# Kernel tuning notes

Hardware: AMD Instinct MI355X
Metric: run time of the kernel (lower is better)

The kernel has to match this reference:

```python
import jax, jax.numpy as jnp
import numpy as np

B, D, T = 32, 6, 2048
FH, ENC, H, CONF, NC, K = 128, 128, 256, 64, 10, 5


def setup_inputs() -> dict:
    key = jax.random.key(0)
    ks = iter(jax.random.split(key, 40))
    n = lambda shape, s=0.05: jax.random.normal(next(ks), shape, dtype=jnp.float32) * s
    inp = {
        'M': jax.random.normal(next(ks), (B, D, T), dtype=jnp.float32),
        # causal conv frontend (4 dilated convs, kernel 5)
        'conv_w0': n((FH, D, K)), 'conv_b0': n((FH,)),
        'conv_w1': n((FH, FH, K)), 'conv_b1': n((FH,)),
        'conv_w2': n((FH, FH, K)), 'conv_b2': n((FH,)),
        'conv_w3': n((FH, FH, K)), 'conv_b3': n((FH,)),
        # encoder projection
        'enc_w': n((ENC, FH)), 'enc_b': n((ENC,)),
        # selective state space
        'A': n((H, H), 0.01), 'ip_w': n((H, ENC)), 'ip_b': n((H,)),
        'state_bias': jnp.zeros((H,), jnp.float32),
        'op_w': n((H, H)), 'op_b': n((H,)),
        # classifier head
        'cls_w1': n((256, H)), 'cls_b1': n((256,)),
        'cls_w2': n((NC, 256)), 'cls_b2': n((NC,)),
        # metanet: 2*D -> 64 -> 128 -> confound_dim
        'mn_w1': n((64, 2 * D)), 'mn_b1': n((64,)),
        'mn_w2': n((128, 64)), 'mn_b2': n((128,)),
        'mn_w3': n((CONF, 128)), 'mn_b3': n((CONF,)),
        # frontdoor: confound_dim -> 128 -> ssm_hidden
        'fd_w1': n((128, CONF)), 'fd_b1': n((128,)),
        'fd_w2': n((H, 128)), 'fd_b2': n((H,)),
    }
    return inp


def _causal_conv(x, w, b, d):
    # x: (B,C,T), w: (O,I,K). pad-left (K-1)*d == pad-both + trim-right in torch code
    y = jax.lax.conv_general_dilated(
        x, w, window_strides=(1,), padding=[((w.shape[2] - 1) * d, 0)],
        rhs_dilation=(d,), dimension_numbers=('NCH', 'OIH', 'NCH'))
    return jax.nn.relu(y + b[None, :, None])


def reference(M, conv_w0, conv_b0, conv_w1, conv_b1, conv_w2, conv_b2, conv_w3, conv_b3,
              enc_w, enc_b, A, ip_w, ip_b, state_bias, op_w, op_b,
              cls_w1, cls_b1, cls_w2, cls_b2,
              mn_w1, mn_b1, mn_w2, mn_b2, mn_w3, mn_b3,
              fd_w1, fd_b1, fd_w2, fd_b2):
    # frontend: 4 causal dilated convs with ReLU
    out = M
    for w, b, d in ((conv_w0, conv_b0, 1), (conv_w1, conv_b1, 2),
                    (conv_w2, conv_b2, 4), (conv_w3, conv_b3, 8)):
        out = _causal_conv(out, w, b, d)
    feat = jnp.einsum('bct,ec->bte', out, enc_w) + enc_b  # (B,T,ENC)
    # SSM: precompute input projection, then sequential scan over T
    u = jnp.einsum('bte,he->bth', feat, ip_w) + ip_b + state_bias  # (B,T,H)

    def step(h, ut):
        h = jax.nn.gelu(h @ A.T + ut, approximate=False)
        return h, h

    h0 = jnp.zeros((M.shape[0], A.shape[0]), M.dtype)
    _, hs = jax.lax.scan(step, h0, jnp.swapaxes(u, 0, 1))  # hs: (T,B,H)
    ssm_out = jnp.einsum('tbh,gh->btg', hs, op_w) + op_b  # (B,T,H)
    pooled = ssm_out.mean(axis=1)  # (B,H)
    logits = jax.nn.relu(pooled @ cls_w1.T + cls_b1) @ cls_w2.T + cls_b2
    # confounder summary: mean & unbiased std over time
    s = jnp.concatenate([M.mean(axis=2), jnp.std(M, axis=2, ddof=1)], axis=1)
    z = jax.nn.relu(s @ mn_w1.T + mn_b1)
    z = jax.nn.relu(z @ mn_w2.T + mn_b2)
    conf_hat = z @ mn_w3.T + mn_b3
    adj = jax.nn.relu(conf_hat @ fd_w1.T + fd_b1) @ fd_w2.T + fd_b2
    corrected = pooled - adj
    return (logits, pooled, corrected, conf_hat)
```

## Files before the change

### kernel.cpp

```cpp
#include <hip/hip_runtime.h>
#include <cmath>


typedef __bf16 bf16_t;
typedef bf16_t bf16x8 __attribute__((ext_vector_type(8)));
typedef float f32x4 __attribute__((ext_vector_type(4)));

__device__ __forceinline__ f32x4 mfma16(bf16x8 a, bf16x8 b, f32x4 c) {
  return __builtin_amdgcn_mfma_f32_16x16x32_bf16(a, b, c, 0, 0, 0);
}

__device__ __forceinline__ float gelu_f(float x) {
  float a = x * 0.70710678118654752440f;
  float z = fabsf(a);
  float t = __builtin_amdgcn_rcpf(1.0f + 0.3275911f * z);
  float p = t * (0.254829592f +
            t * (-0.284496736f +
            t * (1.421413741f +
            t * (-1.453152027f +
            t * 1.061405429f))));
  float e = __expf(-z * z);
  float erf_a = __builtin_copysignf(1.0f - p * e, a);
  return 0.5f * x * (1.0f + erf_a);
}

__global__ void k_prep(const float* __restrict__ w0, const float* __restrict__ w1,
                       const float* __restrict__ w2, const float* __restrict__ w3,
                       const float* __restrict__ ip_w, const float* __restrict__ enc_w,
                       const float* __restrict__ enc_b, const float* __restrict__ ip_b,
                       const float* __restrict__ sbias,
                       bf16_t* __restrict__ wb0, bf16_t* __restrict__ wb1,
                       bf16_t* __restrict__ wb2, bf16_t* __restrict__ wb3,
                       bf16_t* __restrict__ wce, float* __restrict__ bce) {
  int bid = blockIdx.x;
  if (bid >= 976) {
    int idx = (bid - 976) * 256 + threadIdx.x;
    int h = idx >> 7, c = idx & 127;
    float s = 0.f;
    for (int e = 0; e < 128; ++e) s += ip_w[h * 128 + e] * enc_w[e * 128 + c];
    wce[h * 128 + c] = (bf16_t)s;
    if (c == 0) {
      float bv = 0.f;
      for (int e = 0; e < 128; ++e) bv += ip_w[h * 128 + e] * enc_b[e];
      bce[h] = bv + ip_b[h] + sbias[h];
    }
    return;
  }
  int idx = bid * 256 + threadIdx.x;
  if (idx < 128 * 32) {
    int o = idx >> 5, k = idx & 31;
    float v = 0.f;
    if (k < 30) { int i = k / 5, kk = k - i * 5; v = w0[(o * 6 + i) * 5 + kk]; }
    wb0[idx] = (bf16_t)v;
    return;
  }
  int e = idx - 128 * 32;
  if (e < 3 * 5 * 128 * 128) {
    int layer = e / (5 * 128 * 128);
    int r = e - layer * (5 * 128 * 128);
    int ks = r / 16384;
    int o = (r >> 7) & 127;
    int i = r & 127;
    const float* w = layer == 0 ? w1 : layer == 1 ? w2 : w3;
    bf16_t* wb = layer == 0 ? wb1 : layer == 1 ? wb2 : wb3;
    wb[r] = (bf16_t)w[(o * 128 + i) * 5 + ks];
  }
}

__global__ __launch_bounds__(256) void k_conv0(const float* __restrict__ M,
                                               const bf16_t* __restrict__ wb0,
                                               const float* __restrict__ b0,
                                               bf16_t* __restrict__ out) {
  __shared__ float raw[6][136];
  __shared__ bf16_t Xe[128 * 40];
  const int tid = threadIdx.x;
  const int b = blockIdx.y, t0 = blockIdx.x * 128;
  for (int id = tid; id < 6 * 132; id += 256) {
    int i = id / 132, j = id - i * 132;
    int t = t0 - 4 + j;
    raw[i][j] = (t >= 0) ? M[((size_t)b * 6 + i) * 2048 + t] : 0.f;
  }
  __syncthreads();
  for (int id = tid; id < 128 * 32; id += 256) {
    int tl = id >> 5, k = id & 31;
    float v = 0.f;
    if (k < 30) { int i = k / 5, kk = k - i * 5; v = raw[i][tl + kk]; }
    Xe[tl * 40 + k] = (bf16_t)v;
  }
  __syncthreads();
  const int w = tid >> 6, lane = tid & 63, q = lane >> 4, l15 = lane & 15;
  const int k0 = q * 8;
  const f32x4 z4 = {0.f, 0.f, 0.f, 0.f};
  f32x4 acc[2][8];
#pragma unroll
  for (int mt = 0; mt < 2; ++mt)
#pragma unroll
    for (int nt = 0; nt < 8; ++nt) acc[mt][nt] = z4;
  bf16x8 af[2];
#pragma unroll
  for (int mt = 0; mt < 2; ++mt)
    af[mt] = *(const bf16x8*)&Xe[(w * 32 + mt * 16 + l15) * 40 + k0];
#pragma unroll
  for (int nt = 0; nt < 8; ++nt) {
    bf16x8 bf = *(const bf16x8*)&wb0[(nt * 16 + l15) * 32 + k0];
#pragma unroll
    for (int mt = 0; mt < 2; ++mt) acc[mt][nt] = mfma16(af[mt], bf, acc[mt][nt]);
  }
#pragma unroll
  for (int nt = 0; nt < 8; ++nt) {
    const int o = nt * 16 + l15;
    const float bias = b0[o];
#pragma unroll
    for (int mt = 0; mt < 2; ++mt) {
#pragma unroll
      for (int r = 0; r < 4; ++r) {
        int t = t0 + w * 32 + mt * 16 + q * 4 + r;
        float v = acc[mt][nt][r] + bias;
        out[((size_t)b * 2048 + t) * 128 + o] = (bf16_t)(v > 0.f ? v : 0.f);
      }
    }
  }
}

template <int DIL>
__global__ __launch_bounds__(256) void k_conv(const bf16_t* __restrict__ in,
                                              const bf16_t* __restrict__ wb,
                                              const float* __restrict__ bias,
                                              bf16_t* __restrict__ out) {
  __shared__ bf16_t Xs[160 * 136];
  const int tid = threadIdx.x;
  const int b = blockIdx.y, t0 = blockIdx.x * 128;
  const bf16_t* src = in + (size_t)b * 2048 * 128;
  for (int id = tid; id < 160 * 16; id += 256) {
    int r = id >> 4, ck = id & 15;
    int t = t0 + r - 32;
    int4 v = make_int4(0, 0, 0, 0);
    if (t >= 0) v = *(const int4*)(src + (size_t)t * 128 + ck * 8);
    *(int4*)&Xs[r * 136 + ck * 8] = v;
  }
  __syncthreads();
  const int w = tid >> 6, lane = tid & 63, q = lane >> 4, l15 = lane & 15;
  const f32x4 z4 = {0.f, 0.f, 0.f, 0.f};
  f32x4 acc[2][8];
#pragma unroll
  for (int mt = 0; mt < 2; ++mt)
#pragma unroll
    for (int nt = 0; nt < 8; ++nt) acc[mt][nt] = z4;
#pragma unroll
  for (int ks = 0; ks < 5; ++ks) {
    const int shift = (4 - ks) * DIL;
#pragma unroll
    for (int kt = 0; kt < 4; ++kt) {
      const int k0 = kt * 32 + q * 8;
      bf16x8 af[2];
#pragma unroll
      for (int mt = 0; mt < 2; ++mt)
        af[mt] = *(const bf16x8*)&Xs[(32 + w * 32 + mt * 16 + l15 - shift) * 136 + k0];
#pragma unroll
      for (int nt = 0; nt < 8; ++nt) {
        bf16x8 bf = *(const bf16x8*)&wb[((size_t)ks * 128 + nt * 16 + l15) * 128 + k0];
#pragma unroll
        for (int mt = 0; mt < 2; ++mt) acc[mt][nt] = mfma16(af[mt], bf, acc[mt][nt]);
      }
    }
  }
#pragma unroll
  for (int nt = 0; nt < 8; ++nt) {
    const int o = nt * 16 + l15;
    const float bv = bias[o];
#pragma unroll
    for (int mt = 0; mt < 2; ++mt) {
#pragma unroll
      for (int r = 0; r < 4; ++r) {
        int t = t0 + w * 32 + mt * 16 + q * 4 + r;
        float v = acc[mt][nt][r] + bv;
        out[((size_t)b * 2048 + t) * 128 + o] = (bf16_t)(v > 0.f ? v : 0.f);
      }
    }
  }
}

__global__ __launch_bounds__(256) void k_ugemm(const bf16_t* __restrict__ in,
                                               const bf16_t* __restrict__ wce,
                                               const float* __restrict__ bce,
                                               bf16_t* __restrict__ u) {
  __shared__ bf16_t Xs[128 * 136];
  const int tid = threadIdx.x;
  const int b = blockIdx.y, t0 = blockIdx.x * 128, hh = blockIdx.z;
  const bf16_t* src = in + (size_t)b * 2048 * 128;
  for (int id = tid; id < 128 * 16; id += 256) {
    int r = id >> 4, ck = id & 15;
    *(int4*)&Xs[r * 136 + ck * 8] = *(const int4*)(src + (size_t)(t0 + r) * 128 + ck * 8);
  }
  __syncthreads();
  const int w = tid >> 6, lane = tid & 63, q = lane >> 4, l15 = lane & 15;
  const f32x4 z4 = {0.f, 0.f, 0.f, 0.f};
  f32x4 acc[2][8];
#pragma unroll
  for (int mt = 0; mt < 2; ++mt)
#pragma unroll
    for (int nt = 0; nt < 8; ++nt) acc[mt][nt] = z4;
#pragma unroll
  for (int kt = 0; kt < 4; ++kt) {
    const int k0 = kt * 32 + q * 8;
    bf16x8 af[2];
#pragma unroll
    for (int mt = 0; mt < 2; ++mt)
      af[mt] = *(const bf16x8*)&Xs[(w * 32 + mt * 16 + l15) * 136 + k0];
#pragma unroll
    for (int nt = 0; nt < 8; ++nt) {
      bf16x8 bf = *(const bf16x8*)&wce[((size_t)hh * 128 + nt * 16 + l15) * 128 + k0];
#pragma unroll
      for (int mt = 0; mt < 2; ++mt) acc[mt][nt] = mfma16(af[mt], bf, acc[mt][nt]);
    }
  }
#pragma unroll
  for (int nt = 0; nt < 8; ++nt) {
    const int h = hh * 128 + nt * 16 + l15;
    const float bv = bce[h];
#pragma unroll
    for (int mt = 0; mt < 2; ++mt) {
#pragma unroll
      for (int r = 0; r < 4; ++r) {
        int t = t0 + w * 32 + mt * 16 + q * 4 + r;
        u[((size_t)b * 2048 + t) * 256 + h] = (bf16_t)(acc[mt][nt][r] + bv);
      }
    }
  }
}

__global__ __launch_bounds__(1024, 1) void k_scan(const float* __restrict__ Am,
                                                  const bf16_t* __restrict__ u,
                                                  float* __restrict__ hbarOut) {
  __shared__ bf16_t hb[2][256];
  const int b = blockIdx.x;
  const int tid = threadIdx.x;
  const int w = tid >> 6, lane = tid & 63, q = lane >> 4, l15 = lane & 15;
  const int c = w * 16 + l15;

  bf16x8 bfr[8];
#pragma unroll
  for (int kt = 0; kt < 8; ++kt) {
    const float* ap = Am + (size_t)c * 256 + kt * 32 + q * 8;
    f32x4 p0 = *(const f32x4*)ap;
    f32x4 p1 = *(const f32x4*)(ap + 4);
    bf16x8 v;
    v[0] = (bf16_t)p0[0]; v[1] = (bf16_t)p0[1]; v[2] = (bf16_t)p0[2]; v[3] = (bf16_t)p0[3];
    v[4] = (bf16_t)p1[0]; v[5] = (bf16_t)p1[1]; v[6] = (bf16_t)p1[2]; v[7] = (bf16_t)p1[3];
    bfr[kt] = v;
  }
  if (tid < 256) {
    hb[0][tid] = (bf16_t)0.f;
    hb[1][tid] = (bf16_t)0.f;
  }
  const bf16_t* up = u + (size_t)b * 2048 * 256 + c;
  float hbar = 0.f;
  bf16_t ua = up[0];
  bf16_t ub = up[256];
  __syncthreads();

  const f32x4 z4 = {0.f, 0.f, 0.f, 0.f};

#define SCAN_STEP(RD, WR, UREG)                                   \
  {                                                               \
    bf16x8 af[8];                                                 \
    _Pragma("unroll")                                             \
    for (int kt = 0; kt < 8; ++kt)                                \
      af[kt] = *(const bf16x8*)&hb[RD][kt * 32 + q * 8];          \
    float uin = (float)(UREG);                                    \
    f32x4 acc = z4;                                               \
    acc[0] = uin;                                                 \
    _Pragma("unroll")                                             \
    for (int kt = 0; kt < 8; ++kt)                                \
      acc = mfma16(af[kt], bfr[kt], acc);                         \
    __builtin_amdgcn_sched_group_barrier(0x100, 8, 0);            \
    __builtin_amdgcn_sched_group_barrier(0x008, 8, 0);            \
    float g = gelu_f(acc[0]);                                     \
    if (q == 0) hb[WR][c] = (bf16_t)g;                            \
    asm volatile("s_waitcnt lgkmcnt(0)" ::: "memory");            \
    __builtin_amdgcn_s_barrier();                                 \
    __builtin_amdgcn_sched_barrier(0);                            \
    hbar += g;                                                    \
  }

  for (int t = 0; t < 2048; t += 2) {
    bf16_t ua2 = (t + 2 < 2048) ? up[(size_t)(t + 2) * 256] : (bf16_t)0.f;
    SCAN_STEP(0, 1, ua)
    bf16_t ub2 = (t + 3 < 2048) ? up[(size_t)(t + 3) * 256] : (bf16_t)0.f;
    SCAN_STEP(1, 0, ub)
    ua = ua2;
    ub = ub2;
  }
#undef SCAN_STEP

  if (q == 0) hbarOut[b * 256 + c] = hbar * (1.f / 2048.f);
}

__global__ __launch_bounds__(256) void k_post(
    const float* __restrict__ M, const float* __restrict__ hbar,
    const float* __restrict__ w1, const float* __restrict__ b1,
    const float* __restrict__ w2, const float* __restrict__ b2,
    const float* __restrict__ w3, const float* __restrict__ b3,
    const float* __restrict__ f1, const float* __restrict__ fb1,
    const float* __restrict__ f2, const float* __restrict__ fb2,
    const float* __restrict__ op_w, const float* __restrict__ op_b,
    const float* __restrict__ cw1, const float* __restrict__ cb1,
    const float* __restrict__ cw2, const float* __restrict__ cb2,
    float* __restrict__ out) {
  const int b = blockIdx.x, tid = threadIdx.x;
  const int w = tid >> 6, lane = tid & 63;
  __shared__ float s12[12], z1[64], z2[128], ch[64], a1[128], adjs[256];
  __shared__ float hs[256], ps[256], hid[256];
  __shared__ float as_[4], ass_[4];
  for (int c = 0; c < 6; ++c) {
    const float* p = M + ((size_t)b * 6 + c) * 2048;
    float s = 0.f, ss = 0.f;
    for (int t = tid; t < 2048; t += 256) { float v = p[t]; s += v; ss += v * v; }
    for (int o = 32; o > 0; o >>= 1) { s += __shfl_down(s, o, 64); ss += __shfl_down(ss, o, 64); }
    if (lane == 0) { as_[w] = s; ass_[w] = ss; }
    __syncthreads();
    if (tid == 0) {
      s = as_[0] + as_[1] + as_[2] + as_[3];
      ss = ass_[0] + ass_[1] + ass_[2] + ass_[3];
      float mean = s * (1.f / 2048.f);
      float var = (ss - 2048.f * mean * mean) * (1.f / 2047.f);
      if (var < 0.f) var = 0.f;
      s12[c] = mean;
      s12[6 + c] = sqrtf(var);
    }
    __syncthreads();
  }
  if (tid < 64) {
    float v = b1[tid];
    for (int e = 0; e < 12; ++e) v += w1[tid * 12 + e] * s12[e];
    z1[tid] = v > 0.f ? v : 0.f;
  }
  __syncthreads();
  if (tid < 128) {
    float v = b2[tid];
    for (int e = 0; e < 64; ++e) v += w2[tid * 64 + e] * z1[e];
    z2[tid] = v > 0.f ? v : 0.f;
  }
  __syncthreads();
  if (tid < 64) {
    float v = b3[tid];
    for (int e = 0; e < 128; ++e) v += w3[tid * 128 + e] * z2[e];
    ch[tid] = v;
    out[16704 + b * 64 + tid] = v;
  }
  __syncthreads();
  if (tid < 128) {
    float v = fb1[tid];
    for (int e = 0; e < 64; ++e) v += f1[tid * 64 + e] * ch[e];
    a1[tid] = v > 0.f ? v : 0.f;
  }
  __syncthreads();
  {
    float v = fb2[tid];
    for (int e = 0; e < 128; ++e) v += f2[tid * 128 + e] * a1[e];
    adjs[tid] = v;
  }
  hs[tid] = hbar[b * 256 + tid];
  __syncthreads();
  float v = op_b[tid];
  for (int h = 0; h < 256; ++h) v += op_w[tid * 256 + h] * hs[h];
  out[320 + b * 256 + tid] = v;
  out[8512 + b * 256 + tid] = v - adjs[tid];
  ps[tid] = v;
  __syncthreads();
  float hv = cb1[tid];
  for (int h = 0; h < 256; ++h) hv += cw1[tid * 256 + h] * ps[h];
  hid[tid] = hv > 0.f ? hv : 0.f;
  __syncthreads();
  if (tid < 10) {
    float lv = cb2[tid];
    for (int h = 0; h < 256; ++h) lv += cw2[tid * 256 + h] * hid[h];
    out[b * 10 + tid] = lv;
  }
}

extern "C" void kernel_launch(void* const* d_in, const int* in_sizes, int n_in,
                              void* d_out, int out_size, void* d_ws, size_t ws_size,
                              hipStream_t stream) {
  (void)in_sizes; (void)n_in; (void)out_size; (void)ws_size;
  const float* M    = (const float*)d_in[0];
  const float* w0   = (const float*)d_in[1];  const float* b0  = (const float*)d_in[2];
  const float* w1   = (const float*)d_in[3];  const float* b1  = (const float*)d_in[4];
  const float* w2   = (const float*)d_in[5];  const float* b2  = (const float*)d_in[6];
  const float* w3   = (const float*)d_in[7];  const float* b3  = (const float*)d_in[8];
  const float* encw = (const float*)d_in[9];  const float* encb = (const float*)d_in[10];
  const float* Am   = (const float*)d_in[11];
  const float* ipw  = (const float*)d_in[12]; const float* ipb = (const float*)d_in[13];
  const float* sb   = (const float*)d_in[14];
  const float* opw  = (const float*)d_in[15]; const float* opb = (const float*)d_in[16];
  const float* cw1  = (const float*)d_in[17]; const float* cb1 = (const float*)d_in[18];
  const float* cw2  = (const float*)d_in[19]; const float* cb2 = (const float*)d_in[20];
  const float* mw1  = (const float*)d_in[21]; const float* mb1 = (const float*)d_in[22];
  const float* mw2  = (const float*)d_in[23]; const float* mb2 = (const float*)d_in[24];
  const float* mw3  = (const float*)d_in[25]; const float* mb3 = (const float*)d_in[26];
  const float* fw1  = (const float*)d_in[27]; const float* fb1 = (const float*)d_in[28];
  const float* fw2  = (const float*)d_in[29]; const float* fb2 = (const float*)d_in[30];
  float* out = (float*)d_out;

  char* ws = (char*)d_ws;
  bf16_t* wb0  = (bf16_t*)(ws + 0);
  bf16_t* wb1  = (bf16_t*)(ws + 8192);
  bf16_t* wb2  = (bf16_t*)(ws + 172032);
  bf16_t* wb3  = (bf16_t*)(ws + 335872);
  bf16_t* wce  = (bf16_t*)(ws + 499712);
  float*  bce  = (float*) (ws + 565248);
  float*  hbar = (float*) (ws + 566272);
  bf16_t* actA = (bf16_t*)(ws + 633856);
  bf16_t* actB = (bf16_t*)(ws + 17411072);
  bf16_t* u    = (bf16_t*)(ws + 34188288);

  k_prep<<<1104, 256, 0, stream>>>(w0, w1, w2, w3, ipw, encw, encb, ipb, sb,
                                   wb0, wb1, wb2, wb3, wce, bce);
  k_conv0<<<dim3(16, 32), 256, 0, stream>>>(M, wb0, b0, actA);
  k_conv<2><<<dim3(16, 32), 256, 0, stream>>>(actA, wb1, b1, actB);
  k_conv<4><<<dim3(16, 32), 256, 0, stream>>>(actB, wb2, b2, actA);
  k_conv<8><<<dim3(16, 32), 256, 0, stream>>>(actA, wb3, b3, actB);
  k_ugemm<<<dim3(16, 32, 2), 256, 0, stream>>>(actB, wce, bce, u);
  k_scan<<<32, 1024, 0, stream>>>(Am, u, hbar);
  k_post<<<32, 256, 0, stream>>>(M, hbar, mw1, mb1, mw2, mb2, mw3, mb3,
                                 fw1, fb1, fw2, fb2, opw, opb,
                                 cw1, cb1, cw2, cb2, out);
}
```

Measured before the change: 1.465 ms.

## Replace MFMA scan step with per-thread fp16 dot2 row products

The sequential SSM scan now runs 256 threads per batch, one per output state, instead of 1024 threads. Each thread holds its whole row of A in registers as fp16 and computes the matvec with v_dot2_f32_f16 over the shared hidden state, which is now stored in fp16 rather than bf16. This removes the MFMA latency chain and the 16-lane replication on every time step, and lets the per-step barrier cover four waves instead of sixteen. In exchange each thread issues 128 dot instructions serially per step, keeps 128 registers of A, and the fp16 range and precision differ from bf16.

```diff
diff --git a/kernel.cpp b/kernel.cpp
--- a/kernel.cpp
+++ b/kernel.cpp
@@ -5,9 +5,21 @@
 typedef __bf16 bf16_t;
 typedef bf16_t bf16x8 __attribute__((ext_vector_type(8)));
 typedef float f32x4 __attribute__((ext_vector_type(4)));
+typedef _Float16 f16_t;
+typedef f16_t f16x2 __attribute__((ext_vector_type(2)));
+typedef f16_t f16x8 __attribute__((ext_vector_type(8)));
 
 __device__ __forceinline__ f32x4 mfma16(bf16x8 a, bf16x8 b, f32x4 c) {
   return __builtin_amdgcn_mfma_f32_16x16x32_bf16(a, b, c, 0, 0, 0);
+}
+
+__device__ __forceinline__ float fdot2(f16x2 a, f16x2 b, float c) {
+#if __has_builtin(__builtin_amdgcn_fdot2)
+  return __builtin_amdgcn_fdot2(a, b, c, false);
+#else
+  asm("v_dot2_f32_f16 %0, %1, %2, %0" : "+v"(c) : "v"(a), "v"(b));
+  return c;
+#endif
 }
 
 __device__ __forceinline__ float gelu_f(float x) {
@@ -229,54 +241,49 @@
   }
 }
 
-__global__ __launch_bounds__(1024, 1) void k_scan(const float* __restrict__ Am,
-                                                  const bf16_t* __restrict__ u,
-                                                  float* __restrict__ hbarOut) {
-  __shared__ bf16_t hb[2][256];
+__global__ __launch_bounds__(256, 1) void k_scan(const float* __restrict__ Am,
+                                                 const bf16_t* __restrict__ u,
+                                                 float* __restrict__ hbarOut) {
+  __shared__ f16_t hb[2][256];
   const int b = blockIdx.x;
-  const int tid = threadIdx.x;
-  const int w = tid >> 6, lane = tid & 63, q = lane >> 4, l15 = lane & 15;
-  const int c = w * 16 + l15;
-
-  bf16x8 bfr[8];
-#pragma unroll
-  for (int kt = 0; kt < 8; ++kt) {
-    const float* ap = Am + (size_t)c * 256 + kt * 32 + q * 8;
-    f32x4 p0 = *(const f32x4*)ap;
-    f32x4 p1 = *(const f32x4*)(ap + 4);
-    bf16x8 v;
-    v[0] = (bf16_t)p0[0]; v[1] = (bf16_t)p0[1]; v[2] = (bf16_t)p0[2]; v[3] = (bf16_t)p0[3];
-    v[4] = (bf16_t)p1[0]; v[5] = (bf16_t)p1[1]; v[6] = (bf16_t)p1[2]; v[7] = (bf16_t)p1[3];
-    bfr[kt] = v;
-  }
-  if (tid < 256) {
-    hb[0][tid] = (bf16_t)0.f;
-    hb[1][tid] = (bf16_t)0.f;
-  }
+  const int c = threadIdx.x;
+
+  f16x8 Ac[32];
+#pragma unroll
+  for (int k8 = 0; k8 < 32; ++k8) {
+    const float* ap = Am + (size_t)c * 256 + k8 * 8;
+    f16x8 v;
+#pragma unroll
+    for (int e = 0; e < 8; ++e) v[e] = (f16_t)ap[e];
+    Ac[k8] = v;
+  }
+  hb[0][c] = (f16_t)0.f;
+  hb[1][c] = (f16_t)0.f;
   const bf16_t* up = u + (size_t)b * 2048 * 256 + c;
   float hbar = 0.f;
   bf16_t ua = up[0];
   bf16_t ub = up[256];
   __syncthreads();
 
-  const f32x4 z4 = {0.f, 0.f, 0.f, 0.f};
-
 #define SCAN_STEP(RD, WR, UREG)                                   \
   {                                                               \
-    bf16x8 af[8];                                                 \
+    float a0 = 0.f, a1 = 0.f, a2 = 0.f, a3 = 0.f;                 \
     _Pragma("unroll")                                             \
-    for (int kt = 0; kt < 8; ++kt)                                \
-      af[kt] = *(const bf16x8*)&hb[RD][kt * 32 + q * 8];          \
-    float uin = (float)(UREG);                                    \
-    f32x4 acc = z4;                                               \
-    acc[0] = uin;                                                 \
-    _Pragma("unroll")                                             \
-    for (int kt = 0; kt < 8; ++kt)                                \
-      acc = mfma16(af[kt], bfr[kt], acc);                         \
-    __builtin_amdgcn_sched_group_barrier(0x100, 8, 0);            \
-    __builtin_amdgcn_sched_group_barrier(0x008, 8, 0);            \
-    float g = gelu_f(acc[0]);                                     \
-    if (q == 0) hb[WR][c] = (bf16_t)g;                            \
+    for (int k8 = 0; k8 < 32; ++k8) {                             \
+      f16x8 h8 = *(const f16x8*)&hb[RD][k8 * 8];                  \
+      f16x8 A8 = Ac[k8];                                          \
+      f16x2 ha = {h8[0], h8[1]}, Aa = {A8[0], A8[1]};             \
+      f16x2 hbp = {h8[2], h8[3]}, Ab = {A8[2], A8[3]};            \
+      f16x2 hc = {h8[4], h8[5]}, Acp = {A8[4], A8[5]};            \
+      f16x2 hd = {h8[6], h8[7]}, Ad = {A8[6], A8[7]};             \
+      a0 = fdot2(Aa, ha, a0);                                     \
+      a1 = fdot2(Ab, hbp, a1);                                    \
+      a2 = fdot2(Acp, hc, a2);                                    \
+      a3 = fdot2(Ad, hd, a3);                                     \
+    }                                                             \
+    float y = ((a0 + a1) + (a2 + a3)) + (float)(UREG);            \
+    float g = gelu_f(y);                                          \
+    hb[WR][c] = (f16_t)g;                                         \
     asm volatile("s_waitcnt lgkmcnt(0)" ::: "memory");            \
     __builtin_amdgcn_s_barrier();                                 \
     __builtin_amdgcn_sched_barrier(0);                            \
@@ -293,7 +300,7 @@
   }
 #undef SCAN_STEP
 
-  if (q == 0) hbarOut[b * 256 + c] = hbar * (1.f / 2048.f);
+  hbarOut[b * 256 + c] = hbar * (1.f / 2048.f);
 }
 
 __global__ __launch_bounds__(256) void k_post(
@@ -421,7 +428,7 @@
   k_conv<4><<<dim3(16, 32), 256, 0, stream>>>(actB, wb2, b2, actA);
   k_conv<8><<<dim3(16, 32), 256, 0, stream>>>(actA, wb3, b3, actB);
   k_ugemm<<<dim3(16, 32, 2), 256, 0, stream>>>(actB, wce, bce, u);
-  k_scan<<<32, 1024, 0, stream>>>(Am, u, hbar);
+  k_scan<<<32, 256, 0, stream>>>(Am, u, hbar);
   k_post<<<32, 256, 0, stream>>>(M, hbar, mw1, mb1, mw2, mb2, mw3, mb3,
                                  fw1, fb1, fw2, fb2, opw, opb,
                                  cw1, cb1, cw2, cb2, out);
```

Measured after the change: 1.744 ms. 1.19x slower.
